# Kernel optimization log

Hardware: AMD Instinct MI355X
Metric: run time of the kernel (lower is better)

Reference implementation:

```python
import jax, jax.numpy as jnp
import numpy as np

N = 50000      # nodes
E = 800000     # edges (avg degree 16)
D_IN = 128     # in_feats
D_H = 128      # n_hidden
D_OUT = 64     # n_classes


def _lin(k, fan_in, fan_out):
    # torch nn.Linear default init: U(-1/sqrt(fan_in), 1/sqrt(fan_in))
    s = 1.0 / np.sqrt(fan_in)
    return jax.random.uniform(k, (fan_in, fan_out), jnp.float32, -s, s)


def setup_inputs() -> dict:
    key = jax.random.key(0)
    ks = jax.random.split(key, 12)
    return {
        "x": jax.random.normal(ks[0], (N, D_IN), jnp.float32),
        "edge_src": jax.random.randint(ks[1], (E,), 0, N, jnp.int32),
        "edge_dst": jax.random.randint(ks[2], (E,), 0, N, jnp.int32),
        # layer 0: in_feats -> n_hidden
        "W_self0": _lin(ks[3], D_IN, D_H),
        "W_neigh0": _lin(ks[4], D_IN, D_H),
        "b0": jnp.zeros((D_H,), jnp.float32),
        # layer 1: n_hidden -> n_hidden
        "W_self1": _lin(ks[5], D_H, D_H),
        "W_neigh1": _lin(ks[6], D_H, D_H),
        "b1": jnp.zeros((D_H,), jnp.float32),
        # layer 2: n_hidden -> n_classes
        "W_self2": _lin(ks[7], D_H, D_OUT),
        "W_neigh2": _lin(ks[8], D_H, D_OUT),
        "b2": jnp.zeros((D_OUT,), jnp.float32),
    }


def _sage_conv(x, src, dst, W_self, W_neigh, b):
    """DGL SAGEConv with 'mean' aggregator:
    out = x @ W_self + mean_{u in N(v)} x_u @ W_neigh + b
    Zero in-degree nodes get zero neighbor term (degree clamped to 1)."""
    n = x.shape[0]
    agg = jax.ops.segment_sum(x[src], dst, num_segments=n)          # [N, d]
    deg = jax.ops.segment_sum(jnp.ones((src.shape[0],), x.dtype), dst,
                              num_segments=n)                        # [N]
    h_neigh = agg / jnp.maximum(deg, 1.0)[:, None]
    return x @ W_self + h_neigh @ W_neigh + b


def reference(x, edge_src, edge_dst,
              W_self0, W_neigh0, b0,
              W_self1, W_neigh1, b1,
              W_self2, W_neigh2, b2):
    # dropout is identity in eval/inference mode
    h = jax.nn.relu(_sage_conv(x, edge_src, edge_dst, W_self0, W_neigh0, b0))
    h = jax.nn.relu(_sage_conv(h, edge_src, edge_dst, W_self1, W_neigh1, b1))
    return _sage_conv(h, edge_src, edge_dst, W_self2, W_neigh2, b2)
```

## Files before the change

### kernel.cpp

```cpp
#include <hip/hip_runtime.h>

#define NN 50000
#define NPAD 50048
#define NE 800000
#define CAP 64
#define NSLICE 6250

#define EBG 391
#define EDGE_BLOCKS (EBG * 8)
#define CVT_BLOCKS 782
#define W_BLOCKS 320
#define PREP_GRID (EDGE_BLOCKS + CVT_BLOCKS + W_BLOCKS)

typedef _Float16 f16;
typedef _Float16 f16x8 __attribute__((ext_vector_type(8)));
typedef float f32x4 __attribute__((ext_vector_type(4)));
typedef unsigned short u16;
typedef unsigned short u16x4 __attribute__((ext_vector_type(4)));
typedef unsigned short u16x8 __attribute__((ext_vector_type(8)));

__global__ __launch_bounds__(256) void prep_kernel(
    const float* __restrict__ X, const int* __restrict__ esrc,
    const int* __restrict__ edst,
    const float* __restrict__ WS0, const float* __restrict__ WN0,
    const float* __restrict__ WS1, const float* __restrict__ WN1,
    const float* __restrict__ WS2, const float* __restrict__ WN2,
    f16* __restrict__ XH, f16* __restrict__ wt0, f16* __restrict__ wt1,
    f16* __restrict__ wt2, int* __restrict__ cursor, u16* __restrict__ eidx) {
    const int bid = blockIdx.x;
    if (bid < EDGE_BLOCKS) {
        const int g = bid & 7;
        const int gi = bid >> 3;
        const int lo = g * NSLICE, hi = lo + NSLICE;
        const int per = (NE + EBG - 1) / EBG;
        const int s = gi * per;
        const int e_end = (s + per < NE) ? s + per : NE;
        for (int e = s + threadIdx.x; e < e_end; e += 256) {
            int d = edst[e];
            if (d >= lo && d < hi) {
                int p = atomicAdd(&cursor[d], 1);
                if (p < CAP) eidx[(d << 6) + p] = (u16)esrc[e];
            }
        }
    } else if (bid < EDGE_BLOCKS + CVT_BLOCKS) {
        const int total8 = NN * 128 / 8;
        int t = (bid - EDGE_BLOCKS) * 256 + threadIdx.x;
        for (int i = t; i < total8; i += CVT_BLOCKS * 256) {
            float4 v0 = *reinterpret_cast<const float4*>(X + (size_t)i * 8);
            float4 v1 = *reinterpret_cast<const float4*>(X + (size_t)i * 8 + 4);
            f16x8 o = {(f16)v0.x, (f16)v0.y, (f16)v0.z, (f16)v0.w,
                       (f16)v1.x, (f16)v1.y, (f16)v1.z, (f16)v1.w};
            *reinterpret_cast<f16x8*>(XH + (size_t)i * 8) = o;
        }
    } else {
        int t = (bid - EDGE_BLOCKS - CVT_BLOCKS) * 256 + threadIdx.x;
        if (t < 32768) {
            int j = t >> 8, k = t & 255;
            float v = (k < 128) ? WS0[k * 128 + j] : WN0[(k - 128) * 128 + j];
            wt0[j * 256 + k] = (f16)v;
        } else if (t < 65536) {
            int u = t - 32768;
            int j = u >> 8, k = u & 255;
            float v = (k < 128) ? WS1[k * 128 + j] : WN1[(k - 128) * 128 + j];
            wt1[j * 256 + k] = (f16)v;
        } else if (t < 81920) {
            int u = t - 65536;
            int j = u >> 7, k = u & 127;
            float v = (j < 64) ? WS2[k * 64 + j] : WN2[k * 64 + (j - 64)];
            wt2[j * 128 + k] = (f16)v;
        }
    }
}

__global__ __launch_bounds__(512) void fused_layer(const f16* __restrict__ X,
                                                   const int* __restrict__ cnt_,
                                                   const u16* __restrict__ eidx,
                                                   const f16* __restrict__ WT,
                                                   const float* __restrict__ BIAS,
                                                   f16* __restrict__ O16, int n) {
    __shared__ f16 hmt[128 * 128];
    const int lane = threadIdx.x & 63;
    const int wid = threadIdx.x >> 6;
    const int rowbase = blockIdx.x * 128;

    {
        const int sl = lane & 15;
#pragma unroll 2
        for (int it = 0; it < 4; it++) {
            int nl = wid * 16 + it * 4 + (lane >> 4);
            int node = rowbase + nl;
            float acc[8];
#pragma unroll
            for (int j = 0; j < 8; j++) acc[j] = 0.f;
            int cdeg = 0;
            if (node < n) {
                cdeg = cnt_[node];
                int cnt = cdeg < CAP ? cdeg : CAP;
                const u16* row = eidx + ((size_t)node << 6);
                int e = 0;
                for (; e + 8 <= cnt; e += 8) {
                    u16x8 s8 = *reinterpret_cast<const u16x8*>(row + e);
                    f16x8 v0 = *reinterpret_cast<const f16x8*>(X + (size_t)s8[0] * 128 + sl * 8);
                    f16x8 v1 = *reinterpret_cast<const f16x8*>(X + (size_t)s8[1] * 128 + sl * 8);
                    f16x8 v2 = *reinterpret_cast<const f16x8*>(X + (size_t)s8[2] * 128 + sl * 8);
                    f16x8 v3 = *reinterpret_cast<const f16x8*>(X + (size_t)s8[3] * 128 + sl * 8);
                    f16x8 v4 = *reinterpret_cast<const f16x8*>(X + (size_t)s8[4] * 128 + sl * 8);
                    f16x8 v5 = *reinterpret_cast<const f16x8*>(X + (size_t)s8[5] * 128 + sl * 8);
                    f16x8 v6 = *reinterpret_cast<const f16x8*>(X + (size_t)s8[6] * 128 + sl * 8);
                    f16x8 v7 = *reinterpret_cast<const f16x8*>(X + (size_t)s8[7] * 128 + sl * 8);
#pragma unroll
                    for (int j = 0; j < 8; j++)
                        acc[j] += (((float)v0[j] + (float)v1[j]) + ((float)v2[j] + (float)v3[j])) +
                                  (((float)v4[j] + (float)v5[j]) + ((float)v6[j] + (float)v7[j]));
                }
                for (; e + 4 <= cnt; e += 4) {
                    u16x4 s4 = *reinterpret_cast<const u16x4*>(row + e);
                    f16x8 v0 = *reinterpret_cast<const f16x8*>(X + (size_t)s4[0] * 128 + sl * 8);
                    f16x8 v1 = *reinterpret_cast<const f16x8*>(X + (size_t)s4[1] * 128 + sl * 8);
                    f16x8 v2 = *reinterpret_cast<const f16x8*>(X + (size_t)s4[2] * 128 + sl * 8);
                    f16x8 v3 = *reinterpret_cast<const f16x8*>(X + (size_t)s4[3] * 128 + sl * 8);
#pragma unroll
                    for (int j = 0; j < 8; j++)
                        acc[j] += ((float)v0[j] + (float)v1[j]) + ((float)v2[j] + (float)v3[j]);
                }
                for (; e < cnt; e++) {
                    int s0 = row[e];
                    f16x8 v0 = *reinterpret_cast<const f16x8*>(X + (size_t)s0 * 128 + sl * 8);
#pragma unroll
                    for (int j = 0; j < 8; j++) acc[j] += (float)v0[j];
                }
            }
            float iv = 1.0f / fmaxf((float)cdeg, 1.0f);
            f16x8 o;
#pragma unroll
            for (int j = 0; j < 8; j++) o[j] = (f16)(acc[j] * iv);
            int chunk = sl ^ (nl & 7);
            *reinterpret_cast<f16x8*>(hmt + nl * 128 + chunk * 8) = o;
        }
    }
    __syncthreads();

    constexpr int MT = 4, NT = 2;
    const int rh = wid >> 2;
    const int n0 = (wid & 3) * 32;
    const int ar = lane & 15;
    const int kq = lane >> 4;
    const int kg = kq * 8;

    f32x4 acc[MT][NT];
#pragma unroll
    for (int mt = 0; mt < MT; mt++)
#pragma unroll
        for (int nt = 0; nt < NT; nt++) acc[mt][nt] = (f32x4){0.f, 0.f, 0.f, 0.f};

#pragma unroll
    for (int k0 = 0; k0 < 256; k0 += 32) {
        f16x8 a[MT], b[NT];
#pragma unroll
        for (int mt = 0; mt < MT; mt++) {
            const int rl = rh * 64 + mt * 16 + ar;
            if (k0 < 128) {
                a[mt] = *reinterpret_cast<const f16x8*>(
                    X + (size_t)(rowbase + rl) * 128 + k0 + kg);
            } else {
                int chunk = ((k0 - 128) >> 3) + kq;
                a[mt] = *reinterpret_cast<const f16x8*>(
                    hmt + rl * 128 + (chunk ^ (rl & 7)) * 8);
            }
        }
#pragma unroll
        for (int nt = 0; nt < NT; nt++)
            b[nt] = *reinterpret_cast<const f16x8*>(
                WT + (size_t)(n0 + nt * 16 + ar) * 256 + k0 + kg);
#pragma unroll
        for (int mt = 0; mt < MT; mt++)
#pragma unroll
            for (int nt = 0; nt < NT; nt++)
                acc[mt][nt] = __builtin_amdgcn_mfma_f32_16x16x32_f16(
                    a[mt], b[nt], acc[mt][nt], 0, 0, 0);
    }

    const int orow = (lane >> 4) * 4;
    const int ocol = lane & 15;
#pragma unroll
    for (int nt = 0; nt < NT; nt++) {
        const int col = n0 + nt * 16 + ocol;
        const float bias = BIAS[col];
#pragma unroll
        for (int mt = 0; mt < MT; mt++) {
#pragma unroll
            for (int j = 0; j < 4; j++) {
                int row = rowbase + rh * 64 + mt * 16 + orow + j;
                if (row < n) {
                    float v = fmaxf(acc[mt][nt][j] + bias, 0.f);
                    O16[(size_t)row * 128 + col] = (f16)v;
                }
            }
        }
    }
}

__global__ __launch_bounds__(256) void gemm2(const f16* __restrict__ A1,
                                             const f16* __restrict__ WT,
                                             const float* __restrict__ BIAS,
                                             f16* __restrict__ O16, int n) {
    constexpr int MT = 4, NT = 4;
    const int lane = threadIdx.x & 63;
    const int wid = threadIdx.x >> 6;
    const int m0 = blockIdx.x * 128 + (wid >> 1) * 64;
    const int n0 = (wid & 1) * 64;
    const int ar = lane & 15;
    const int kg = (lane >> 4) * 8;

    f32x4 acc[MT][NT];
#pragma unroll
    for (int mt = 0; mt < MT; mt++)
#pragma unroll
        for (int nt = 0; nt < NT; nt++) acc[mt][nt] = (f32x4){0.f, 0.f, 0.f, 0.f};

#pragma unroll
    for (int k0 = 0; k0 < 128; k0 += 32) {
        f16x8 a[MT], b[NT];
#pragma unroll
        for (int mt = 0; mt < MT; mt++)
            a[mt] = *reinterpret_cast<const f16x8*>(
                A1 + (size_t)(m0 + mt * 16 + ar) * 128 + k0 + kg);
#pragma unroll
        for (int nt = 0; nt < NT; nt++)
            b[nt] = *reinterpret_cast<const f16x8*>(
                WT + (size_t)(n0 + nt * 16 + ar) * 128 + k0 + kg);
#pragma unroll
        for (int mt = 0; mt < MT; mt++)
#pragma unroll
            for (int nt = 0; nt < NT; nt++)
                acc[mt][nt] = __builtin_amdgcn_mfma_f32_16x16x32_f16(
                    a[mt], b[nt], acc[mt][nt], 0, 0, 0);
    }

    const int orow = (lane >> 4) * 4;
    const int ocol = lane & 15;
#pragma unroll
    for (int nt = 0; nt < NT; nt++) {
        const int col = n0 + nt * 16 + ocol;
        const float bias = (col < 64) ? BIAS[col] : 0.f;
#pragma unroll
        for (int mt = 0; mt < MT; mt++) {
#pragma unroll
            for (int j = 0; j < 4; j++) {
                int row = m0 + mt * 16 + orow + j;
                if (row < n)
                    O16[(size_t)row * 128 + col] = (f16)(acc[mt][nt][j] + bias);
            }
        }
    }
}

__global__ __launch_bounds__(256) void gather_out(const f16* __restrict__ Y,
                                                  const int* __restrict__ cnt_,
                                                  const u16* __restrict__ eidx,
                                                  float* __restrict__ OUT, int n) {
    int wave = blockIdx.x * 4 + (threadIdx.x >> 6);
    int lane = threadIdx.x & 63;
    int node = wave * 8 + (lane >> 3);
    int sl = lane & 7;
    if (node >= n) return;
    int cdeg = cnt_[node];
    int cnt = cdeg < CAP ? cdeg : CAP;
    const u16* row = eidx + ((size_t)node << 6);
    float acc[8];
#pragma unroll
    for (int j = 0; j < 8; j++) acc[j] = 0.f;
    int e = 0;
    for (; e + 8 <= cnt; e += 8) {
        u16x8 s8 = *reinterpret_cast<const u16x8*>(row + e);
        f16x8 v0 = *reinterpret_cast<const f16x8*>(Y + (size_t)s8[0] * 128 + 64 + sl * 8);
        f16x8 v1 = *reinterpret_cast<const f16x8*>(Y + (size_t)s8[1] * 128 + 64 + sl * 8);
        f16x8 v2 = *reinterpret_cast<const f16x8*>(Y + (size_t)s8[2] * 128 + 64 + sl * 8);
        f16x8 v3 = *reinterpret_cast<const f16x8*>(Y + (size_t)s8[3] * 128 + 64 + sl * 8);
        f16x8 v4 = *reinterpret_cast<const f16x8*>(Y + (size_t)s8[4] * 128 + 64 + sl * 8);
        f16x8 v5 = *reinterpret_cast<const f16x8*>(Y + (size_t)s8[5] * 128 + 64 + sl * 8);
        f16x8 v6 = *reinterpret_cast<const f16x8*>(Y + (size_t)s8[6] * 128 + 64 + sl * 8);
        f16x8 v7 = *reinterpret_cast<const f16x8*>(Y + (size_t)s8[7] * 128 + 64 + sl * 8);
#pragma unroll
        for (int j = 0; j < 8; j++)
            acc[j] += (((float)v0[j] + (float)v1[j]) + ((float)v2[j] + (float)v3[j])) +
                      (((float)v4[j] + (float)v5[j]) + ((float)v6[j] + (float)v7[j]));
    }
    for (; e + 4 <= cnt; e += 4) {
        u16x4 s4 = *reinterpret_cast<const u16x4*>(row + e);
        f16x8 v0 = *reinterpret_cast<const f16x8*>(Y + (size_t)s4[0] * 128 + 64 + sl * 8);
        f16x8 v1 = *reinterpret_cast<const f16x8*>(Y + (size_t)s4[1] * 128 + 64 + sl * 8);
        f16x8 v2 = *reinterpret_cast<const f16x8*>(Y + (size_t)s4[2] * 128 + 64 + sl * 8);
        f16x8 v3 = *reinterpret_cast<const f16x8*>(Y + (size_t)s4[3] * 128 + 64 + sl * 8);
#pragma unroll
        for (int j = 0; j < 8; j++)
            acc[j] += ((float)v0[j] + (float)v1[j]) + ((float)v2[j] + (float)v3[j]);
    }
    for (; e < cnt; e++) {
        int s0 = row[e];
        f16x8 v0 = *reinterpret_cast<const f16x8*>(Y + (size_t)s0 * 128 + 64 + sl * 8);
#pragma unroll
        for (int j = 0; j < 8; j++) acc[j] += (float)v0[j];
    }
    float iv = 1.0f / fmaxf((float)cdeg, 1.0f);
    f16x8 self = *reinterpret_cast<const f16x8*>(Y + (size_t)node * 128 + sl * 8);
    float o[8];
#pragma unroll
    for (int j = 0; j < 8; j++) o[j] = acc[j] * iv + (float)self[j];
    float* dst = OUT + (size_t)node * 64 + sl * 8;
    *reinterpret_cast<float4*>(dst) = *reinterpret_cast<float4*>(o);
    *reinterpret_cast<float4*>(dst + 4) = *reinterpret_cast<float4*>(o + 4);
}

extern "C" void kernel_launch(void* const* d_in, const int* in_sizes, int n_in,
                              void* d_out, int out_size, void* d_ws, size_t ws_size,
                              hipStream_t stream) {
    const float* x        = (const float*)d_in[0];
    const int*   esrc     = (const int*)d_in[1];
    const int*   edst     = (const int*)d_in[2];
    const float* W_self0  = (const float*)d_in[3];
    const float* W_neigh0 = (const float*)d_in[4];
    const float* b0       = (const float*)d_in[5];
    const float* W_self1  = (const float*)d_in[6];
    const float* W_neigh1 = (const float*)d_in[7];
    const float* b1       = (const float*)d_in[8];
    const float* W_self2  = (const float*)d_in[9];
    const float* W_neigh2 = (const float*)d_in[10];
    const float* b2       = (const float*)d_in[11];
    float* out = (float*)d_out;

    char* ws = (char*)d_ws;
    auto align1k = [](size_t v) { return (v + 1023) & ~(size_t)1023; };
    size_t off = 0;
    int* cursor = (int*)(ws + off); off = align1k(off + (size_t)NN * 4);
    u16* eidx   = (u16*)(ws + off); off = align1k(off + (size_t)NN * CAP * 2);
    f16* wt0    = (f16*)(ws + off); off = align1k(off + (size_t)128 * 256 * 2);
    f16* wt1    = (f16*)(ws + off); off = align1k(off + (size_t)128 * 256 * 2);
    f16* wt2    = (f16*)(ws + off); off = align1k(off + (size_t)128 * 128 * 2);
    const size_t FEAT16 = (size_t)NPAD * 128 * 2;
    f16* xh = (f16*)(ws + off); off += FEAT16;
    f16* h0 = (f16*)(ws + off); off += FEAT16;
    f16* h1 = (f16*)(ws + off); off += FEAT16;
    f16* yc = (f16*)(ws + off); off += FEAT16;

    const int n = NN;
    const int g8blocks = (n + 31) / 32;
    const int tile_blocks = NPAD / 128;

    hipMemsetAsync(cursor, 0, (size_t)n * sizeof(int), stream);
    prep_kernel<<<PREP_GRID, 256, 0, stream>>>(x, esrc, edst,
                                               W_self0, W_neigh0, W_self1, W_neigh1,
                                               W_self2, W_neigh2,
                                               xh, wt0, wt1, wt2, cursor, eidx);

    fused_layer<<<tile_blocks, 512, 0, stream>>>(xh, cursor, eidx, wt0, b0, h0, n);
    fused_layer<<<tile_blocks, 512, 0, stream>>>(h0, cursor, eidx, wt1, b1, h1, n);
    gemm2<<<tile_blocks, 256, 0, stream>>>(h1, wt2, b2, yc, n);
    gather_out<<<g8blocks, 256, 0, stream>>>(yc, cursor, eidx, out, n);
}
```

Baseline: 184.9 us.

## Bucket edges by source slice and gather slice-by-slice in lockstep for cache locality

Edges are now binned per destination into 8 source-range slices of at most 16 entries each. The gather loops walk the slices in order, with a block-wide barrier after each slice, so every wave in a block reads from the same source-row region at the same time. This is meant to raise L2/MALL hit rates on the random feature gathers. gemm2 also switches to 64-row tiles to launch more blocks. The cost is 8x more cursor atomics, memory and memset, extra barriers, and the per-slice cap of 16 risks dropping edges on skewed inputs.

Result: slower. 329.6 us (+78.3%).

```diff
diff --git a/kernel.cpp b/kernel.cpp
--- a/kernel.cpp
+++ b/kernel.cpp
@@ -3,7 +3,9 @@
 #define NN 50000
 #define NPAD 50048
 #define NE 800000
-#define CAP 64
+#define NSL 8
+#define SCAP 16
+#define SLICE_W 6250
 #define NSLICE 6250
 
 #define EBG 391
@@ -38,8 +40,10 @@
         for (int e = s + threadIdx.x; e < e_end; e += 256) {
             int d = edst[e];
             if (d >= lo && d < hi) {
-                int p = atomicAdd(&cursor[d], 1);
-                if (p < CAP) eidx[(d << 6) + p] = (u16)esrc[e];
+                int src = esrc[e];
+                int slice = src / SLICE_W;
+                int p = atomicAdd(&cursor[(d << 3) + slice], 1);
+                if (p < SCAP) eidx[(d << 7) + (slice << 4) + p] = (u16)src;
             }
         }
     } else if (bid < EDGE_BLOCKS + CVT_BLOCKS) {
@@ -82,61 +86,80 @@
     const int lane = threadIdx.x & 63;
     const int wid = threadIdx.x >> 6;
     const int rowbase = blockIdx.x * 128;
-
-    {
-        const int sl = lane & 15;
-#pragma unroll 2
+    const int sl = lane & 15;
+    const int ng = lane >> 4;
+
+    float acc[4][8];
+    int cdeg[4];
+    int nodes[4];
+#pragma unroll
+    for (int it = 0; it < 4; it++) {
+        int nl = wid * 16 + it * 4 + ng;
+        nodes[it] = rowbase + nl;
+#pragma unroll
+        for (int j = 0; j < 8; j++) acc[it][j] = 0.f;
+        int cd = 0;
+        if (nodes[it] < n) {
+            int4 ca = *reinterpret_cast<const int4*>(cnt_ + ((size_t)nodes[it] << 3));
+            int4 cb = *reinterpret_cast<const int4*>(cnt_ + ((size_t)nodes[it] << 3) + 4);
+            cd = ((ca.x + ca.y) + (ca.z + ca.w)) + ((cb.x + cb.y) + (cb.z + cb.w));
+        }
+        cdeg[it] = cd;
+    }
+
+    for (int p = 0; p < NSL; p++) {
+#pragma unroll
         for (int it = 0; it < 4; it++) {
-            int nl = wid * 16 + it * 4 + (lane >> 4);
-            int node = rowbase + nl;
-            float acc[8];
-#pragma unroll
-            for (int j = 0; j < 8; j++) acc[j] = 0.f;
-            int cdeg = 0;
-            if (node < n) {
-                cdeg = cnt_[node];
-                int cnt = cdeg < CAP ? cdeg : CAP;
-                const u16* row = eidx + ((size_t)node << 6);
-                int e = 0;
-                for (; e + 8 <= cnt; e += 8) {
-                    u16x8 s8 = *reinterpret_cast<const u16x8*>(row + e);
-                    f16x8 v0 = *reinterpret_cast<const f16x8*>(X + (size_t)s8[0] * 128 + sl * 8);
-                    f16x8 v1 = *reinterpret_cast<const f16x8*>(X + (size_t)s8[1] * 128 + sl * 8);
-                    f16x8 v2 = *reinterpret_cast<const f16x8*>(X + (size_t)s8[2] * 128 + sl * 8);
-                    f16x8 v3 = *reinterpret_cast<const f16x8*>(X + (size_t)s8[3] * 128 + sl * 8);
-                    f16x8 v4 = *reinterpret_cast<const f16x8*>(X + (size_t)s8[4] * 128 + sl * 8);
-                    f16x8 v5 = *reinterpret_cast<const f16x8*>(X + (size_t)s8[5] * 128 + sl * 8);
-                    f16x8 v6 = *reinterpret_cast<const f16x8*>(X + (size_t)s8[6] * 128 + sl * 8);
-                    f16x8 v7 = *reinterpret_cast<const f16x8*>(X + (size_t)s8[7] * 128 + sl * 8);
-#pragma unroll
-                    for (int j = 0; j < 8; j++)
-                        acc[j] += (((float)v0[j] + (float)v1[j]) + ((float)v2[j] + (float)v3[j])) +
+            int node = nodes[it];
+            if (node >= n) continue;
+            int cnt = cnt_[(node << 3) + p];
+            cnt = cnt < SCAP ? cnt : SCAP;
+            const u16* bk = eidx + (((size_t)node << 7) + (p << 4));
+            int e = 0;
+            for (; e + 8 <= cnt; e += 8) {
+                u16x8 s8 = *reinterpret_cast<const u16x8*>(bk + e);
+                f16x8 v0 = *reinterpret_cast<const f16x8*>(X + (size_t)s8[0] * 128 + sl * 8);
+                f16x8 v1 = *reinterpret_cast<const f16x8*>(X + (size_t)s8[1] * 128 + sl * 8);
+                f16x8 v2 = *reinterpret_cast<const f16x8*>(X + (size_t)s8[2] * 128 + sl * 8);
+                f16x8 v3 = *reinterpret_cast<const f16x8*>(X + (size_t)s8[3] * 128 + sl * 8);
+                f16x8 v4 = *reinterpret_cast<const f16x8*>(X + (size_t)s8[4] * 128 + sl * 8);
+                f16x8 v5 = *reinterpret_cast<const f16x8*>(X + (size_t)s8[5] * 128 + sl * 8);
+                f16x8 v6 = *reinterpret_cast<const f16x8*>(X + (size_t)s8[6] * 128 + sl * 8);
+                f16x8 v7 = *reinterpret_cast<const f16x8*>(X + (size_t)s8[7] * 128 + sl * 8);
+#pragma unroll
+                for (int j = 0; j < 8; j++)
+                    acc[it][j] += (((float)v0[j] + (float)v1[j]) + ((float)v2[j] + (float)v3[j])) +
                                   (((float)v4[j] + (float)v5[j]) + ((float)v6[j] + (float)v7[j]));
-                }
-                for (; e + 4 <= cnt; e += 4) {
-                    u16x4 s4 = *reinterpret_cast<const u16x4*>(row + e);
-                    f16x8 v0 = *reinterpret_cast<const f16x8*>(X + (size_t)s4[0] * 128 + sl * 8);
-                    f16x8 v1 = *reinterpret_cast<const f16x8*>(X + (size_t)s4[1] * 128 + sl * 8);
-                    f16x8 v2 = *reinterpret_cast<const f16x8*>(X + (size_t)s4[2] * 128 + sl * 8);
-                    f16x8 v3 = *reinterpret_cast<const f16x8*>(X + (size_t)s4[3] * 128 + sl * 8);
-#pragma unroll
-                    for (int j = 0; j < 8; j++)
-                        acc[j] += ((float)v0[j] + (float)v1[j]) + ((float)v2[j] + (float)v3[j]);
-                }
-                for (; e < cnt; e++) {
-                    int s0 = row[e];
-                    f16x8 v0 = *reinterpret_cast<const f16x8*>(X + (size_t)s0 * 128 + sl * 8);
-#pragma unroll
-                    for (int j = 0; j < 8; j++) acc[j] += (float)v0[j];
-                }
-            }
-            float iv = 1.0f / fmaxf((float)cdeg, 1.0f);
-            f16x8 o;
-#pragma unroll
-            for (int j = 0; j < 8; j++) o[j] = (f16)(acc[j] * iv);
-            int chunk = sl ^ (nl & 7);
-            *reinterpret_cast<f16x8*>(hmt + nl * 128 + chunk * 8) = o;
-        }
+            }
+            if (e + 4 <= cnt) {
+                u16x4 s4 = *reinterpret_cast<const u16x4*>(bk + e);
+                f16x8 v0 = *reinterpret_cast<const f16x8*>(X + (size_t)s4[0] * 128 + sl * 8);
+                f16x8 v1 = *reinterpret_cast<const f16x8*>(X + (size_t)s4[1] * 128 + sl * 8);
+                f16x8 v2 = *reinterpret_cast<const f16x8*>(X + (size_t)s4[2] * 128 + sl * 8);
+                f16x8 v3 = *reinterpret_cast<const f16x8*>(X + (size_t)s4[3] * 128 + sl * 8);
+#pragma unroll
+                for (int j = 0; j < 8; j++)
+                    acc[it][j] += ((float)v0[j] + (float)v1[j]) + ((float)v2[j] + (float)v3[j]);
+                e += 4;
+            }
+            for (; e < cnt; e++) {
+                int s0 = bk[e];
+                f16x8 v0 = *reinterpret_cast<const f16x8*>(X + (size_t)s0 * 128 + sl * 8);
+#pragma unroll
+                for (int j = 0; j < 8; j++) acc[it][j] += (float)v0[j];
+            }
+        }
+        __syncthreads();
+    }
+
+#pragma unroll
+    for (int it = 0; it < 4; it++) {
+        int nl = wid * 16 + it * 4 + ng;
+        float iv = 1.0f / fmaxf((float)cdeg[it], 1.0f);
+        f16x8 o;
+#pragma unroll
+        for (int j = 0; j < 8; j++) o[j] = (f16)(acc[it][j] * iv);
+        *reinterpret_cast<f16x8*>(hmt + nl * 128 + ((sl ^ (nl & 7)) << 3)) = o;
     }
     __syncthreads();
 
@@ -147,11 +170,11 @@
     const int kq = lane >> 4;
     const int kg = kq * 8;
 
-    f32x4 acc[MT][NT];
+    f32x4 gacc[MT][NT];
 #pragma unroll
     for (int mt = 0; mt < MT; mt++)
 #pragma unroll
-        for (int nt = 0; nt < NT; nt++) acc[mt][nt] = (f32x4){0.f, 0.f, 0.f, 0.f};
+        for (int nt = 0; nt < NT; nt++) gacc[mt][nt] = (f32x4){0.f, 0.f, 0.f, 0.f};
 
 #pragma unroll
     for (int k0 = 0; k0 < 256; k0 += 32) {
@@ -176,8 +199,8 @@
         for (int mt = 0; mt < MT; mt++)
 #pragma unroll
             for (int nt = 0; nt < NT; nt++)
-                acc[mt][nt] = __builtin_amdgcn_mfma_f32_16x16x32_f16(
-                    a[mt], b[nt], acc[mt][nt], 0, 0, 0);
+                gacc[mt][nt] = __builtin_amdgcn_mfma_f32_16x16x32_f16(
+                    a[mt], b[nt], gacc[mt][nt], 0, 0, 0);
     }
 
     const int orow = (lane >> 4) * 4;
@@ -192,7 +215,7 @@
             for (int j = 0; j < 4; j++) {
                 int row = rowbase + rh * 64 + mt * 16 + orow + j;
                 if (row < n) {
-                    float v = fmaxf(acc[mt][nt][j] + bias, 0.f);
+                    float v = fmaxf(gacc[mt][nt][j] + bias, 0.f);
                     O16[(size_t)row * 128 + col] = (f16)v;
                 }
             }
@@ -204,10 +227,10 @@
                                              const f16* __restrict__ WT,
                                              const float* __restrict__ BIAS,
                                              f16* __restrict__ O16, int n) {
-    constexpr int MT = 4, NT = 4;
+    constexpr int MT = 2, NT = 4;
     const int lane = threadIdx.x & 63;
     const int wid = threadIdx.x >> 6;
-    const int m0 = blockIdx.x * 128 + (wid >> 1) * 64;
+    const int m0 = blockIdx.x * 64 + (wid >> 1) * 32;
     const int n0 = (wid & 1) * 64;
     const int ar = lane & 15;
     const int kg = (lane >> 4) * 8;
@@ -263,53 +286,69 @@
     int lane = threadIdx.x & 63;
     int node = wave * 8 + (lane >> 3);
     int sl = lane & 7;
-    if (node >= n) return;
-    int cdeg = cnt_[node];
-    int cnt = cdeg < CAP ? cdeg : CAP;
-    const u16* row = eidx + ((size_t)node << 6);
+    const bool act = node < n;
     float acc[8];
 #pragma unroll
     for (int j = 0; j < 8; j++) acc[j] = 0.f;
-    int e = 0;
-    for (; e + 8 <= cnt; e += 8) {
-        u16x8 s8 = *reinterpret_cast<const u16x8*>(row + e);
-        f16x8 v0 = *reinterpret_cast<const f16x8*>(Y + (size_t)s8[0] * 128 + 64 + sl * 8);
-        f16x8 v1 = *reinterpret_cast<const f16x8*>(Y + (size_t)s8[1] * 128 + 64 + sl * 8);
-        f16x8 v2 = *reinterpret_cast<const f16x8*>(Y + (size_t)s8[2] * 128 + 64 + sl * 8);
-        f16x8 v3 = *reinterpret_cast<const f16x8*>(Y + (size_t)s8[3] * 128 + 64 + sl * 8);
-        f16x8 v4 = *reinterpret_cast<const f16x8*>(Y + (size_t)s8[4] * 128 + 64 + sl * 8);
-        f16x8 v5 = *reinterpret_cast<const f16x8*>(Y + (size_t)s8[5] * 128 + 64 + sl * 8);
-        f16x8 v6 = *reinterpret_cast<const f16x8*>(Y + (size_t)s8[6] * 128 + 64 + sl * 8);
-        f16x8 v7 = *reinterpret_cast<const f16x8*>(Y + (size_t)s8[7] * 128 + 64 + sl * 8);
-#pragma unroll
-        for (int j = 0; j < 8; j++)
-            acc[j] += (((float)v0[j] + (float)v1[j]) + ((float)v2[j] + (float)v3[j])) +
-                      (((float)v4[j] + (float)v5[j]) + ((float)v6[j] + (float)v7[j]));
-    }
-    for (; e + 4 <= cnt; e += 4) {
-        u16x4 s4 = *reinterpret_cast<const u16x4*>(row + e);
-        f16x8 v0 = *reinterpret_cast<const f16x8*>(Y + (size_t)s4[0] * 128 + 64 + sl * 8);
-        f16x8 v1 = *reinterpret_cast<const f16x8*>(Y + (size_t)s4[1] * 128 + 64 + sl * 8);
-        f16x8 v2 = *reinterpret_cast<const f16x8*>(Y + (size_t)s4[2] * 128 + 64 + sl * 8);
-        f16x8 v3 = *reinterpret_cast<const f16x8*>(Y + (size_t)s4[3] * 128 + 64 + sl * 8);
-#pragma unroll
-        for (int j = 0; j < 8; j++)
-            acc[j] += ((float)v0[j] + (float)v1[j]) + ((float)v2[j] + (float)v3[j]);
-    }
-    for (; e < cnt; e++) {
-        int s0 = row[e];
-        f16x8 v0 = *reinterpret_cast<const f16x8*>(Y + (size_t)s0 * 128 + 64 + sl * 8);
-#pragma unroll
-        for (int j = 0; j < 8; j++) acc[j] += (float)v0[j];
-    }
-    float iv = 1.0f / fmaxf((float)cdeg, 1.0f);
-    f16x8 self = *reinterpret_cast<const f16x8*>(Y + (size_t)node * 128 + sl * 8);
-    float o[8];
-#pragma unroll
-    for (int j = 0; j < 8; j++) o[j] = acc[j] * iv + (float)self[j];
-    float* dst = OUT + (size_t)node * 64 + sl * 8;
-    *reinterpret_cast<float4*>(dst) = *reinterpret_cast<float4*>(o);
-    *reinterpret_cast<float4*>(dst + 4) = *reinterpret_cast<float4*>(o + 4);
+    int cdeg = 0;
+    if (act) {
+        int4 ca = *reinterpret_cast<const int4*>(cnt_ + ((size_t)node << 3));
+        int4 cb = *reinterpret_cast<const int4*>(cnt_ + ((size_t)node << 3) + 4);
+        cdeg = ((ca.x + ca.y) + (ca.z + ca.w)) + ((cb.x + cb.y) + (cb.z + cb.w));
+    }
+
+    for (int p = 0; p < NSL; p++) {
+        if (act) {
+            int cnt = cnt_[(node << 3) + p];
+            cnt = cnt < SCAP ? cnt : SCAP;
+            const u16* bk = eidx + (((size_t)node << 7) + (p << 4));
+            int e = 0;
+            for (; e + 8 <= cnt; e += 8) {
+                u16x8 s8 = *reinterpret_cast<const u16x8*>(bk + e);
+                f16x8 v0 = *reinterpret_cast<const f16x8*>(Y + (size_t)s8[0] * 128 + 64 + sl * 8);
+                f16x8 v1 = *reinterpret_cast<const f16x8*>(Y + (size_t)s8[1] * 128 + 64 + sl * 8);
+                f16x8 v2 = *reinterpret_cast<const f16x8*>(Y + (size_t)s8[2] * 128 + 64 + sl * 8);
+                f16x8 v3 = *reinterpret_cast<const f16x8*>(Y + (size_t)s8[3] * 128 + 64 + sl * 8);
+                f16x8 v4 = *reinterpret_cast<const f16x8*>(Y + (size_t)s8[4] * 128 + 64 + sl * 8);
+                f16x8 v5 = *reinterpret_cast<const f16x8*>(Y + (size_t)s8[5] * 128 + 64 + sl * 8);
+                f16x8 v6 = *reinterpret_cast<const f16x8*>(Y + (size_t)s8[6] * 128 + 64 + sl * 8);
+                f16x8 v7 = *reinterpret_cast<const f16x8*>(Y + (size_t)s8[7] * 128 + 64 + sl * 8);
+#pragma unroll
+                for (int j = 0; j < 8; j++)
+                    acc[j] += (((float)v0[j] + (float)v1[j]) + ((float)v2[j] + (float)v3[j])) +
+                              (((float)v4[j] + (float)v5[j]) + ((float)v6[j] + (float)v7[j]));
+            }
+            if (e + 4 <= cnt) {
+                u16x4 s4 = *reinterpret_cast<const u16x4*>(bk + e);
+                f16x8 v0 = *reinterpret_cast<const f16x8*>(Y + (size_t)s4[0] * 128 + 64 + sl * 8);
+                f16x8 v1 = *reinterpret_cast<const f16x8*>(Y + (size_t)s4[1] * 128 + 64 + sl * 8);
+                f16x8 v2 = *reinterpret_cast<const f16x8*>(Y + (size_t)s4[2] * 128 + 64 + sl * 8);
+                f16x8 v3 = *reinterpret_cast<const f16x8*>(Y + (size_t)s4[3] * 128 + 64 + sl * 8);
+#pragma unroll
+                for (int j = 0; j < 8; j++)
+                    acc[j] += ((float)v0[j] + (float)v1[j]) + ((float)v2[j] + (float)v3[j]);
+                e += 4;
+            }
+            for (; e < cnt; e++) {
+                int s0 = bk[e];
+                f16x8 v0 = *reinterpret_cast<const f16x8*>(Y + (size_t)s0 * 128 + 64 + sl * 8);
+#pragma unroll
+                for (int j = 0; j < 8; j++) acc[j] += (float)v0[j];
+            }
+        }
+        __syncthreads();
+    }
+
+    if (act) {
+        float iv = 1.0f / fmaxf((float)cdeg, 1.0f);
+        f16x8 self = *reinterpret_cast<const f16x8*>(Y + (size_t)node * 128 + sl * 8);
+        float o[8];
+#pragma unroll
+        for (int j = 0; j < 8; j++) o[j] = acc[j] * iv + (float)self[j];
+        float* dst = OUT + (size_t)node * 64 + sl * 8;
+        *reinterpret_cast<float4*>(dst) = *reinterpret_cast<float4*>(o);
+        *reinterpret_cast<float4*>(dst + 4) = *reinterpret_cast<float4*>(o + 4);
+    }
 }
 
 extern "C" void kernel_launch(void* const* d_in, const int* in_sizes, int n_in,
@@ -332,8 +371,8 @@
     char* ws = (char*)d_ws;
     auto align1k = [](size_t v) { return (v + 1023) & ~(size_t)1023; };
     size_t off = 0;
-    int* cursor = (int*)(ws + off); off = align1k(off + (size_t)NN * 4);
-    u16* eidx   = (u16*)(ws + off); off = align1k(off + (size_t)NN * CAP * 2);
+    int* cursor = (int*)(ws + off); off = align1k(off + (size_t)NN * NSL * 4);
+    u16* eidx   = (u16*)(ws + off); off = align1k(off + (size_t)NN * NSL * SCAP * 2);
     f16* wt0    = (f16*)(ws + off); off = align1k(off + (size_t)128 * 256 * 2);
     f16* wt1    = (f16*)(ws + off); off = align1k(off + (size_t)128 * 256 * 2);
     f16* wt2    = (f16*)(ws + off); off = align1k(off + (size_t)128 * 128 * 2);
@@ -345,16 +384,17 @@
 
     const int n = NN;
     const int g8blocks = (n + 31) / 32;
-    const int tile_blocks = NPAD / 128;
-
-    hipMemsetAsync(cursor, 0, (size_t)n * sizeof(int), stream);
+    const int tile128_blocks = NPAD / 128;
+    const int tile64_blocks = NPAD / 64;
+
+    hipMemsetAsync(cursor, 0, (size_t)NN * NSL * sizeof(int), stream);
     prep_kernel<<<PREP_GRID, 256, 0, stream>>>(x, esrc, edst,
                                                W_self0, W_neigh0, W_self1, W_neigh1,
                                                W_self2, W_neigh2,
                                                xh, wt0, wt1, wt2, cursor, eidx);
 
-    fused_layer<<<tile_blocks, 512, 0, stream>>>(xh, cursor, eidx, wt0, b0, h0, n);
-    fused_layer<<<tile_blocks, 512, 0, stream>>>(h0, cursor, eidx, wt1, b1, h1, n);
-    gemm2<<<tile_blocks, 256, 0, stream>>>(h1, wt2, b2, yc, n);
+    fused_layer<<<tile128_blocks, 512, 0, stream>>>(xh, cursor, eidx, wt0, b0, h0, n);
+    fused_layer<<<tile128_blocks, 512, 0, stream>>>(h0, cursor, eidx, wt1, b1, h1, n);
+    gemm2<<<tile64_blocks, 256, 0, stream>>>(h1, wt2, b2, yc, n);
     gather_out<<<g8blocks, 256, 0, stream>>>(yc, cursor, eidx, out, n);
 }
```
